# Kernel tuning notes

Measured on AMD Instinct MI355X. Metric: run time of the kernel, lower is better.

Reference implementation:

```python
import jax, jax.numpy as jnp
import numpy as np

GRID = 128                      # grid_size per axis
NUM_CELLS = GRID ** 3
INV_CELL = float(GRID)          # 1.0 / cell_size, cell_size = 1/128, origin = 0
N_POINTS = 1_000_000
D_FEAT = 8
# forward window {0,1}^3 -> 8 stencil offsets (linear shape functions)
OFFSETS = np.stack(np.meshgrid(*([np.arange(2)] * 3), indexing='ij'), -1).reshape(-1, 3)


def setup_inputs() -> dict:
    key = jax.random.key(0)
    k1, k2 = jax.random.split(key)
    position_stack = jax.random.uniform(k1, (N_POINTS, 3), dtype=jnp.float32)  # in [0,1)^3
    point_feature = jax.random.normal(k2, (N_POINTS, D_FEAT), dtype=jnp.float32)
    return {"position_stack": position_stack, "point_feature": point_feature}


def reference(position_stack, point_feature):
    offsets = jnp.asarray(OFFSETS, jnp.int32)                 # [8,3]
    # --- partition: hash each point into its grid cell (origin=0) ---
    rel = position_stack * INV_CELL                            # [N,3], continuous grid coords
    base = jnp.floor(rel).astype(jnp.int32)                    # [N,3] base cell (point_hash grid pos)
    # --- p2g (vmap_grid_gather duality): each point scatters to its 8 forward-window nodes ---
    node = base[:, None, :] + offsets[None, :, :]              # [N,8,3]
    # linear hat weights: prod_d (1 - |rel - node|), nonneg since |diff| <= 1
    w = jnp.prod(1.0 - jnp.abs(rel[:, None, :] - node.astype(rel.dtype)), axis=-1)  # [N,8]
    nw = node % GRID                                           # ravel_multi_index mode='wrap'
    hid = (nw[..., 0] * GRID + nw[..., 1]) * GRID + nw[..., 2]  # [N,8] cell hash ids
    contrib = w[..., None] * point_feature[:, None, :]         # [N,8,D]
    grid_feat = jnp.zeros((NUM_CELLS, D_FEAT), point_feature.dtype)
    grid_feat = grid_feat.at[hid.reshape(-1)].add(contrib.reshape(-1, D_FEAT))  # scatter-add
    # --- g2p (vmap_grid_scatter_fori): gather grid values back to points over forward window ---
    point_out = jnp.einsum('nwd,nw->nd', grid_feat[hid], w)    # [N,D]
    return point_out
```

## Files before the change

kernel.cpp:

```cpp
#include <hip/hip_runtime.h>

#define GRIDSZ 128
#define GMASK 127
#define NUM_CELLS (GRIDSZ * GRIDSZ * GRIDSZ)
#define DFEAT 8
#define NPTS 1000000
#define INV_CELL 128.0f

#define SCAN_BLK 256
#define SCAN_ELEMS 8
#define SCAN_TILE (SCAN_BLK * SCAN_ELEMS)
#define NSCAN_BLOCKS (NUM_CELLS / SCAN_TILE)

__global__ __launch_bounds__(256) void hist_kernel(
    const float* __restrict__ pos,
    int* __restrict__ counts)
{
    int n = blockIdx.x * blockDim.x + threadIdx.x;
    if (n >= NPTS) return;
    float px = pos[n * 3 + 0] * INV_CELL;
    float py = pos[n * 3 + 1] * INV_CELL;
    float pz = pos[n * 3 + 2] * INV_CELL;
    int bx = (int)floorf(px), by = (int)floorf(py), bz = (int)floorf(pz);
    int h = ((bx & GMASK) << 14) | ((by & GMASK) << 7) | (bz & GMASK);
    atomicAdd(&counts[h], 1);
}

__global__ __launch_bounds__(SCAN_BLK) void scan_a(
    int* __restrict__ data,
    int* __restrict__ partial)
{
    __shared__ int lds[SCAN_BLK];
    int t = threadIdx.x;
    int base = blockIdx.x * SCAN_TILE + t * SCAN_ELEMS;
    int v[SCAN_ELEMS];
    int s = 0;
#pragma unroll
    for (int i = 0; i < SCAN_ELEMS; ++i) { v[i] = data[base + i]; s += v[i]; }
    lds[t] = s;
    __syncthreads();
    int incl = s;
    for (int off = 1; off < SCAN_BLK; off <<= 1) {
        int tmp = (t >= off) ? lds[t - off] : 0;
        __syncthreads();
        incl += tmp;
        lds[t] = incl;
        __syncthreads();
    }
    int excl = incl - s;
#pragma unroll
    for (int i = 0; i < SCAN_ELEMS; ++i) { data[base + i] = excl; excl += v[i]; }
    if (t == SCAN_BLK - 1) partial[blockIdx.x] = incl;
}

__global__ __launch_bounds__(1024) void scan_b(int* __restrict__ partial)
{
    __shared__ int lds[NSCAN_BLOCKS];
    int t = threadIdx.x;
    int p = partial[t];
    lds[t] = p;
    __syncthreads();
    int incl = p;
    for (int off = 1; off < NSCAN_BLOCKS; off <<= 1) {
        int tmp = (t >= off) ? lds[t - off] : 0;
        __syncthreads();
        incl += tmp;
        lds[t] = incl;
        __syncthreads();
    }
    partial[t] = incl - p;
}

__global__ __launch_bounds__(256) void scan_c(
    int* __restrict__ offsets, const int* __restrict__ partial)
{
    int i = blockIdx.x * blockDim.x + threadIdx.x;
    offsets[i] += partial[i / SCAN_TILE];
}

__global__ __launch_bounds__(256) void scatter_kernel(
    const float* __restrict__ pos,
    const float* __restrict__ feat,
    int* __restrict__ offsets,
    float4* __restrict__ frac_s,
    float4* __restrict__ feat_s,
    int* __restrict__ orig_s)
{
    int n = blockIdx.x * blockDim.x + threadIdx.x;
    if (n >= NPTS) return;
    float px = pos[n * 3 + 0] * INV_CELL;
    float py = pos[n * 3 + 1] * INV_CELL;
    float pz = pos[n * 3 + 2] * INV_CELL;
    int bx = (int)floorf(px), by = (int)floorf(py), bz = (int)floorf(pz);
    float fx = px - (float)bx, fy = py - (float)by, fz = pz - (float)bz;
    int c = ((bx & GMASK) << 14) | ((by & GMASK) << 7) | (bz & GMASK);
    int slot = atomicAdd(&offsets[c], 1);

    const float4* fp = reinterpret_cast<const float4*>(feat + (size_t)n * DFEAT);
    float4 f0 = fp[0];
    float4 f1 = fp[1];
    frac_s[slot] = make_float4(fx, fy, fz, __int_as_float(c));
    feat_s[(size_t)slot * 2 + 0] = f0;
    feat_s[(size_t)slot * 2 + 1] = f1;
    orig_s[slot] = n;
}

__global__ __launch_bounds__(256) void node_gather_kernel(
    const int* __restrict__ offsets_end,
    const float4* __restrict__ frac_s,
    const float4* __restrict__ feat_s,
    float* __restrict__ grid)
{
    int n = blockIdx.x * blockDim.x + threadIdx.x;
    int nz = n & GMASK, ny = (n >> 7) & GMASK, nx = n >> 14;
    float4 a0 = {0.f, 0.f, 0.f, 0.f};
    float4 a1 = {0.f, 0.f, 0.f, 0.f};
#pragma unroll
    for (int oxy = 0; oxy < 4; ++oxy) {
        int ox = oxy >> 1, oy = oxy & 1;
        int bx = (nx - ox) & GMASK, by = (ny - oy) & GMASK;
        int cbase = (bx << 14) | (by << 7);
        int c1 = cbase | nz;
        if (nz > 0) {
            int c0 = c1 - 1;
            int st0 = (c0 == 0) ? 0 : offsets_end[c0 - 1];
            int en0 = offsets_end[c0];
            int en1 = offsets_end[c1];
            for (int j = st0; j < en1; ++j) {
                float4 fr = frac_s[j];
                float wz = (j < en0) ? fr.z : 1.f - fr.z;
                float w = (ox ? fr.x : 1.f - fr.x) * (oy ? fr.y : 1.f - fr.y) * wz;
                float4 f0 = feat_s[(size_t)j * 2 + 0];
                float4 f1 = feat_s[(size_t)j * 2 + 1];
                a0.x += w * f0.x; a0.y += w * f0.y; a0.z += w * f0.z; a0.w += w * f0.w;
                a1.x += w * f1.x; a1.y += w * f1.y; a1.z += w * f1.z; a1.w += w * f1.w;
            }
        } else {
            int c0 = cbase | 127;
            int st0 = offsets_end[c0 - 1];
            int en0 = offsets_end[c0];
            for (int j = st0; j < en0; ++j) {
                float4 fr = frac_s[j];
                float w = (ox ? fr.x : 1.f - fr.x) * (oy ? fr.y : 1.f - fr.y) * fr.z;
                float4 f0 = feat_s[(size_t)j * 2 + 0];
                float4 f1 = feat_s[(size_t)j * 2 + 1];
                a0.x += w * f0.x; a0.y += w * f0.y; a0.z += w * f0.z; a0.w += w * f0.w;
                a1.x += w * f1.x; a1.y += w * f1.y; a1.z += w * f1.z; a1.w += w * f1.w;
            }
            int st1 = (c1 == 0) ? 0 : offsets_end[c1 - 1];
            int en1 = offsets_end[c1];
            for (int j = st1; j < en1; ++j) {
                float4 fr = frac_s[j];
                float w = (ox ? fr.x : 1.f - fr.x) * (oy ? fr.y : 1.f - fr.y) * (1.f - fr.z);
                float4 f0 = feat_s[(size_t)j * 2 + 0];
                float4 f1 = feat_s[(size_t)j * 2 + 1];
                a0.x += w * f0.x; a0.y += w * f0.y; a0.z += w * f0.z; a0.w += w * f0.w;
                a1.x += w * f1.x; a1.y += w * f1.y; a1.z += w * f1.z; a1.w += w * f1.w;
            }
        }
    }
    float4* gp = reinterpret_cast<float4*>(grid + (size_t)n * DFEAT);
    gp[0] = a0;
    gp[1] = a1;
}

__global__ __launch_bounds__(256) void g2p_sorted_kernel(
    const float4* __restrict__ frac_s,
    const int* __restrict__ orig_s,
    const float* __restrict__ grid,
    float* __restrict__ out)
{
    int j = blockIdx.x * blockDim.x + threadIdx.x;
    if (j >= NPTS) return;
    float4 fr = frac_s[j];
    int c = __float_as_int(fr.w);
    int bx = c >> 14, by = (c >> 7) & GMASK, bz = c & GMASK;

    float wx[2] = {1.0f - fr.x, fr.x};
    float wy[2] = {1.0f - fr.y, fr.y};
    float wz[2] = {1.0f - fr.z, fr.z};

    float4 acc0 = {0.f, 0.f, 0.f, 0.f};
    float4 acc1 = {0.f, 0.f, 0.f, 0.f};
#pragma unroll
    for (int o = 0; o < 8; ++o) {
        int ox = (o >> 2) & 1, oy = (o >> 1) & 1, oz = o & 1;
        float w = wx[ox] * wy[oy] * wz[oz];
        int cx = (bx + ox) & GMASK;
        int cy = (by + oy) & GMASK;
        int cz = (bz + oz) & GMASK;
        int hid = (cx << 14) | (cy << 7) | cz;
        const float4* g = reinterpret_cast<const float4*>(grid + (size_t)hid * DFEAT);
        float4 g0 = g[0];
        float4 g1 = g[1];
        acc0.x += w * g0.x; acc0.y += w * g0.y; acc0.z += w * g0.z; acc0.w += w * g0.w;
        acc1.x += w * g1.x; acc1.y += w * g1.y; acc1.z += w * g1.z; acc1.w += w * g1.w;
    }
    int orig = orig_s[j];
    float4* op = reinterpret_cast<float4*>(out + (size_t)orig * DFEAT);
    op[0] = acc0;
    op[1] = acc1;
}

__global__ __launch_bounds__(256) void p2g_atomic_kernel(
    const float* __restrict__ pos,
    const float* __restrict__ feat,
    float* __restrict__ grid)
{
    int n = blockIdx.x * blockDim.x + threadIdx.x;
    if (n >= NPTS) return;
    float px = pos[n * 3 + 0] * INV_CELL;
    float py = pos[n * 3 + 1] * INV_CELL;
    float pz = pos[n * 3 + 2] * INV_CELL;
    int bx = (int)floorf(px), by = (int)floorf(py), bz = (int)floorf(pz);
    float fx = px - (float)bx, fy = py - (float)by, fz = pz - (float)bz;
    const float4* fp = reinterpret_cast<const float4*>(feat + (size_t)n * DFEAT);
    float4 f0 = fp[0];
    float4 f1 = fp[1];
    float f[8] = {f0.x, f0.y, f0.z, f0.w, f1.x, f1.y, f1.z, f1.w};
    float wx[2] = {1.0f - fx, fx};
    float wy[2] = {1.0f - fy, fy};
    float wz[2] = {1.0f - fz, fz};
#pragma unroll
    for (int o = 0; o < 8; ++o) {
        int ox = (o >> 2) & 1, oy = (o >> 1) & 1, oz = o & 1;
        float w = wx[ox] * wy[oy] * wz[oz];
        int cx = (bx + ox) & GMASK, cy = (by + oy) & GMASK, cz = (bz + oz) & GMASK;
        int hid = (cx << 14) | (cy << 7) | cz;
        float* g = grid + (size_t)hid * DFEAT;
#pragma unroll
        for (int d = 0; d < DFEAT; ++d) atomicAdd(g + d, w * f[d]);
    }
}

__global__ __launch_bounds__(256) void g2p_kernel(
    const float* __restrict__ pos,
    const float* __restrict__ grid,
    float* __restrict__ out)
{
    int n = blockIdx.x * blockDim.x + threadIdx.x;
    if (n >= NPTS) return;
    float px = pos[n * 3 + 0] * INV_CELL;
    float py = pos[n * 3 + 1] * INV_CELL;
    float pz = pos[n * 3 + 2] * INV_CELL;
    int bx = (int)floorf(px), by = (int)floorf(py), bz = (int)floorf(pz);
    float fx = px - (float)bx, fy = py - (float)by, fz = pz - (float)bz;
    float wx[2] = {1.0f - fx, fx};
    float wy[2] = {1.0f - fy, fy};
    float wz[2] = {1.0f - fz, fz};
    float4 acc0 = {0.f, 0.f, 0.f, 0.f};
    float4 acc1 = {0.f, 0.f, 0.f, 0.f};
#pragma unroll
    for (int o = 0; o < 8; ++o) {
        int ox = (o >> 2) & 1, oy = (o >> 1) & 1, oz = o & 1;
        float w = wx[ox] * wy[oy] * wz[oz];
        int cx = (bx + ox) & GMASK;
        int cy = (by + oy) & GMASK;
        int cz = (bz + oz) & GMASK;
        int hid = (cx << 14) | (cy << 7) | cz;
        const float4* g = reinterpret_cast<const float4*>(grid + (size_t)hid * DFEAT);
        float4 g0 = g[0];
        float4 g1 = g[1];
        acc0.x += w * g0.x; acc0.y += w * g0.y; acc0.z += w * g0.z; acc0.w += w * g0.w;
        acc1.x += w * g1.x; acc1.y += w * g1.y; acc1.z += w * g1.z; acc1.w += w * g1.w;
    }
    float4* op = reinterpret_cast<float4*>(out + (size_t)n * DFEAT);
    op[0] = acc0;
    op[1] = acc1;
}

extern "C" void kernel_launch(void* const* d_in, const int* in_sizes, int n_in,
                              void* d_out, int out_size, void* d_ws, size_t ws_size,
                              hipStream_t stream) {
    const float* pos  = (const float*)d_in[0];
    const float* feat = (const float*)d_in[1];
    float* out = (float*)d_out;

    char* ws = (char*)d_ws;
    size_t grid_bytes    = (size_t)NUM_CELLS * DFEAT * sizeof(float);
    size_t offsets_bytes = (size_t)NUM_CELLS * sizeof(int);
    size_t frac_bytes    = (size_t)NPTS * sizeof(float4);
    size_t feats_bytes   = (size_t)NPTS * 2 * sizeof(float4);
    size_t orig_bytes    = (size_t)NPTS * sizeof(int);
    size_t partial_bytes = (size_t)NSCAN_BLOCKS * sizeof(int);

    float* grid     = (float*)ws;
    int* offsets    = (int*)(ws + grid_bytes);
    float4* frac_s  = (float4*)(ws + grid_bytes + offsets_bytes);
    float4* feat_s  = (float4*)(ws + grid_bytes + offsets_bytes + frac_bytes);
    int* orig_s     = (int*)(ws + grid_bytes + offsets_bytes + frac_bytes + feats_bytes);
    int* partial    = (int*)(ws + grid_bytes + offsets_bytes + frac_bytes + feats_bytes + orig_bytes);
    size_t needed = grid_bytes + offsets_bytes + frac_bytes + feats_bytes + orig_bytes + partial_bytes;

    int block = 256;
    int nblk_pts = (NPTS + block - 1) / block;
    int nblk_cells = NUM_CELLS / block;

    if (ws_size >= needed) {
        hipMemsetAsync(offsets, 0, offsets_bytes, stream);
        hist_kernel<<<nblk_pts, block, 0, stream>>>(pos, offsets);
        scan_a<<<NSCAN_BLOCKS, SCAN_BLK, 0, stream>>>(offsets, partial);
        scan_b<<<1, NSCAN_BLOCKS, 0, stream>>>(partial);
        scan_c<<<nblk_cells, block, 0, stream>>>(offsets, partial);
        scatter_kernel<<<nblk_pts, block, 0, stream>>>(pos, feat, offsets, frac_s, feat_s, orig_s);
        node_gather_kernel<<<nblk_cells, block, 0, stream>>>(offsets, frac_s, feat_s, grid);
        g2p_sorted_kernel<<<nblk_pts, block, 0, stream>>>(frac_s, orig_s, grid, out);
    } else {
        hipMemsetAsync(grid, 0, grid_bytes, stream);
        p2g_atomic_kernel<<<nblk_pts, block, 0, stream>>>(pos, feat, grid);
        g2p_kernel<<<nblk_pts, block, 0, stream>>>(pos, grid, out);
    }
}
```

Before: 309.2 us.

## Pack sorted point records and grid into fp16/quantized format, fold scan fixup

Sorted point data is packed into a 32-byte record: features as fp16 pairs, fractional coordinates quantized to 16 bits, plus cell id and original index. The grid is stored as fp16 (16 bytes per cell). The scan_c pass is removed and the block partial sums are added on the fly in scatter and node_gather. This cuts memory traffic and one kernel launch, at the cost of reduced precision in features, grid values and weights, which may break tolerance checks.

```diff
diff --git a/kernel.cpp b/kernel.cpp
--- a/kernel.cpp
+++ b/kernel.cpp
@@ -1,4 +1,5 @@
 #include <hip/hip_runtime.h>
+#include <hip/hip_fp16.h>
 
 #define GRIDSZ 128
 #define GMASK 127
@@ -9,8 +10,22 @@
 
 #define SCAN_BLK 256
 #define SCAN_ELEMS 8
-#define SCAN_TILE (SCAN_BLK * SCAN_ELEMS)
+#define SCAN_TILE 2048
+#define SCAN_SHIFT 11
 #define NSCAN_BLOCKS (NUM_CELLS / SCAN_TILE)
+
+__device__ inline unsigned pack2h(float a, float b) {
+    __half2 h = __floats2half2_rn(a, b);
+    union { __half2 h; unsigned u; } cvt; cvt.h = h; return cvt.u;
+}
+__device__ inline float2 unpack2h(unsigned u) {
+    union { unsigned u; __half2 h; } cvt; cvt.u = u;
+    return __half22float2(cvt.h);
+}
+
+__device__ inline int cum(const int* __restrict__ off, const int* __restrict__ partial, int c) {
+    return off[c] + partial[c >> SCAN_SHIFT];
+}
 
 __global__ __launch_bounds__(256) void hist_kernel(
     const float* __restrict__ pos,
@@ -71,20 +86,12 @@
     partial[t] = incl - p;
 }
 
-__global__ __launch_bounds__(256) void scan_c(
-    int* __restrict__ offsets, const int* __restrict__ partial)
-{
-    int i = blockIdx.x * blockDim.x + threadIdx.x;
-    offsets[i] += partial[i / SCAN_TILE];
-}
-
 __global__ __launch_bounds__(256) void scatter_kernel(
     const float* __restrict__ pos,
     const float* __restrict__ feat,
     int* __restrict__ offsets,
-    float4* __restrict__ frac_s,
-    float4* __restrict__ feat_s,
-    int* __restrict__ orig_s)
+    const int* __restrict__ partial,
+    uint4* __restrict__ rec)
 {
     int n = blockIdx.x * blockDim.x + threadIdx.x;
     if (n >= NPTS) return;
@@ -94,22 +101,35 @@
     int bx = (int)floorf(px), by = (int)floorf(py), bz = (int)floorf(pz);
     float fx = px - (float)bx, fy = py - (float)by, fz = pz - (float)bz;
     int c = ((bx & GMASK) << 14) | ((by & GMASK) << 7) | (bz & GMASK);
-    int slot = atomicAdd(&offsets[c], 1);
+    int slot = atomicAdd(&offsets[c], 1) + partial[c >> SCAN_SHIFT];
 
     const float4* fp = reinterpret_cast<const float4*>(feat + (size_t)n * DFEAT);
     float4 f0 = fp[0];
     float4 f1 = fp[1];
-    frac_s[slot] = make_float4(fx, fy, fz, __int_as_float(c));
-    feat_s[(size_t)slot * 2 + 0] = f0;
-    feat_s[(size_t)slot * 2 + 1] = f1;
-    orig_s[slot] = n;
+
+    uint4 A, B;
+    A.x = pack2h(f0.x, f0.y);
+    A.y = pack2h(f0.z, f0.w);
+    A.z = pack2h(f1.x, f1.y);
+    A.w = pack2h(f1.z, f1.w);
+    unsigned qx = min((unsigned)(fx * 65536.0f), 65535u);
+    unsigned qy = min((unsigned)(fy * 65536.0f), 65535u);
+    unsigned qz = min((unsigned)(fz * 65536.0f), 65535u);
+    B.x = qx | (qy << 16);
+    B.y = qz;
+    B.z = (unsigned)c;
+    B.w = (unsigned)n;
+
+    uint4* dst = rec + (size_t)slot * 2;
+    dst[0] = A;
+    dst[1] = B;
 }
 
 __global__ __launch_bounds__(256) void node_gather_kernel(
     const int* __restrict__ offsets_end,
-    const float4* __restrict__ frac_s,
-    const float4* __restrict__ feat_s,
-    float* __restrict__ grid)
+    const int* __restrict__ partial,
+    const uint4* __restrict__ rec,
+    uint4* __restrict__ gridh)
 {
     int n = blockIdx.x * blockDim.x + threadIdx.x;
     int nz = n & GMASK, ny = (n >> 7) & GMASK, nx = n >> 14;
@@ -123,62 +143,86 @@
         int c1 = cbase | nz;
         if (nz > 0) {
             int c0 = c1 - 1;
-            int st0 = (c0 == 0) ? 0 : offsets_end[c0 - 1];
-            int en0 = offsets_end[c0];
-            int en1 = offsets_end[c1];
+            int st0 = (c0 == 0) ? 0 : cum(offsets_end, partial, c0 - 1);
+            int en0 = cum(offsets_end, partial, c0);
+            int en1 = cum(offsets_end, partial, c1);
             for (int j = st0; j < en1; ++j) {
-                float4 fr = frac_s[j];
-                float wz = (j < en0) ? fr.z : 1.f - fr.z;
-                float w = (ox ? fr.x : 1.f - fr.x) * (oy ? fr.y : 1.f - fr.y) * wz;
-                float4 f0 = feat_s[(size_t)j * 2 + 0];
-                float4 f1 = feat_s[(size_t)j * 2 + 1];
-                a0.x += w * f0.x; a0.y += w * f0.y; a0.z += w * f0.z; a0.w += w * f0.w;
-                a1.x += w * f1.x; a1.y += w * f1.y; a1.z += w * f1.z; a1.w += w * f1.w;
+                const uint4* rp = rec + (size_t)j * 2;
+                uint4 A = rp[0];
+                uint4 B = rp[1];
+                float fx = (float)(B.x & 0xffffu) * (1.f / 65536.f);
+                float fy = (float)(B.x >> 16) * (1.f / 65536.f);
+                float fz = (float)(B.y & 0xffffu) * (1.f / 65536.f);
+                float wz = (j < en0) ? fz : 1.f - fz;
+                float w = (ox ? fx : 1.f - fx) * (oy ? fy : 1.f - fy) * wz;
+                float2 p;
+                p = unpack2h(A.x); a0.x += w * p.x; a0.y += w * p.y;
+                p = unpack2h(A.y); a0.z += w * p.x; a0.w += w * p.y;
+                p = unpack2h(A.z); a1.x += w * p.x; a1.y += w * p.y;
+                p = unpack2h(A.w); a1.z += w * p.x; a1.w += w * p.y;
             }
         } else {
             int c0 = cbase | 127;
-            int st0 = offsets_end[c0 - 1];
-            int en0 = offsets_end[c0];
+            int st0 = cum(offsets_end, partial, c0 - 1);
+            int en0 = cum(offsets_end, partial, c0);
             for (int j = st0; j < en0; ++j) {
-                float4 fr = frac_s[j];
-                float w = (ox ? fr.x : 1.f - fr.x) * (oy ? fr.y : 1.f - fr.y) * fr.z;
-                float4 f0 = feat_s[(size_t)j * 2 + 0];
-                float4 f1 = feat_s[(size_t)j * 2 + 1];
-                a0.x += w * f0.x; a0.y += w * f0.y; a0.z += w * f0.z; a0.w += w * f0.w;
-                a1.x += w * f1.x; a1.y += w * f1.y; a1.z += w * f1.z; a1.w += w * f1.w;
+                const uint4* rp = rec + (size_t)j * 2;
+                uint4 A = rp[0];
+                uint4 B = rp[1];
+                float fx = (float)(B.x & 0xffffu) * (1.f / 65536.f);
+                float fy = (float)(B.x >> 16) * (1.f / 65536.f);
+                float fz = (float)(B.y & 0xffffu) * (1.f / 65536.f);
+                float w = (ox ? fx : 1.f - fx) * (oy ? fy : 1.f - fy) * fz;
+                float2 p;
+                p = unpack2h(A.x); a0.x += w * p.x; a0.y += w * p.y;
+                p = unpack2h(A.y); a0.z += w * p.x; a0.w += w * p.y;
+                p = unpack2h(A.z); a1.x += w * p.x; a1.y += w * p.y;
+                p = unpack2h(A.w); a1.z += w * p.x; a1.w += w * p.y;
             }
-            int st1 = (c1 == 0) ? 0 : offsets_end[c1 - 1];
-            int en1 = offsets_end[c1];
+            int st1 = (c1 == 0) ? 0 : cum(offsets_end, partial, c1 - 1);
+            int en1 = cum(offsets_end, partial, c1);
             for (int j = st1; j < en1; ++j) {
-                float4 fr = frac_s[j];
-                float w = (ox ? fr.x : 1.f - fr.x) * (oy ? fr.y : 1.f - fr.y) * (1.f - fr.z);
-                float4 f0 = feat_s[(size_t)j * 2 + 0];
-                float4 f1 = feat_s[(size_t)j * 2 + 1];
-                a0.x += w * f0.x; a0.y += w * f0.y; a0.z += w * f0.z; a0.w += w * f0.w;
-                a1.x += w * f1.x; a1.y += w * f1.y; a1.z += w * f1.z; a1.w += w * f1.w;
+                const uint4* rp = rec + (size_t)j * 2;
+                uint4 A = rp[0];
+                uint4 B = rp[1];
+                float fx = (float)(B.x & 0xffffu) * (1.f / 65536.f);
+                float fy = (float)(B.x >> 16) * (1.f / 65536.f);
+                float fz = (float)(B.y & 0xffffu) * (1.f / 65536.f);
+                float w = (ox ? fx : 1.f - fx) * (oy ? fy : 1.f - fy) * (1.f - fz);
+                float2 p;
+                p = unpack2h(A.x); a0.x += w * p.x; a0.y += w * p.y;
+                p = unpack2h(A.y); a0.z += w * p.x; a0.w += w * p.y;
+                p = unpack2h(A.z); a1.x += w * p.x; a1.y += w * p.y;
+                p = unpack2h(A.w); a1.z += w * p.x; a1.w += w * p.y;
             }
         }
     }
-    float4* gp = reinterpret_cast<float4*>(grid + (size_t)n * DFEAT);
-    gp[0] = a0;
-    gp[1] = a1;
+    uint4 g;
+    g.x = pack2h(a0.x, a0.y);
+    g.y = pack2h(a0.z, a0.w);
+    g.z = pack2h(a1.x, a1.y);
+    g.w = pack2h(a1.z, a1.w);
+    gridh[n] = g;
 }
 
 __global__ __launch_bounds__(256) void g2p_sorted_kernel(
-    const float4* __restrict__ frac_s,
-    const int* __restrict__ orig_s,
-    const float* __restrict__ grid,
+    const uint4* __restrict__ rec,
+    const uint4* __restrict__ gridh,
     float* __restrict__ out)
 {
     int j = blockIdx.x * blockDim.x + threadIdx.x;
     if (j >= NPTS) return;
-    float4 fr = frac_s[j];
-    int c = __float_as_int(fr.w);
+    uint4 B = rec[(size_t)j * 2 + 1];
+    float fx = (float)(B.x & 0xffffu) * (1.f / 65536.f);
+    float fy = (float)(B.x >> 16) * (1.f / 65536.f);
+    float fz = (float)(B.y & 0xffffu) * (1.f / 65536.f);
+    int c = (int)B.z;
+    int orig = (int)B.w;
     int bx = c >> 14, by = (c >> 7) & GMASK, bz = c & GMASK;
 
-    float wx[2] = {1.0f - fr.x, fr.x};
-    float wy[2] = {1.0f - fr.y, fr.y};
-    float wz[2] = {1.0f - fr.z, fr.z};
+    float wx[2] = {1.0f - fx, fx};
+    float wy[2] = {1.0f - fy, fy};
+    float wz[2] = {1.0f - fz, fz};
 
     float4 acc0 = {0.f, 0.f, 0.f, 0.f};
     float4 acc1 = {0.f, 0.f, 0.f, 0.f};
@@ -190,13 +234,13 @@
         int cy = (by + oy) & GMASK;
         int cz = (bz + oz) & GMASK;
         int hid = (cx << 14) | (cy << 7) | cz;
-        const float4* g = reinterpret_cast<const float4*>(grid + (size_t)hid * DFEAT);
-        float4 g0 = g[0];
-        float4 g1 = g[1];
-        acc0.x += w * g0.x; acc0.y += w * g0.y; acc0.z += w * g0.z; acc0.w += w * g0.w;
-        acc1.x += w * g1.x; acc1.y += w * g1.y; acc1.z += w * g1.z; acc1.w += w * g1.w;
-    }
-    int orig = orig_s[j];
+        uint4 g = gridh[hid];
+        float2 p;
+        p = unpack2h(g.x); acc0.x += w * p.x; acc0.y += w * p.y;
+        p = unpack2h(g.y); acc0.z += w * p.x; acc0.w += w * p.y;
+        p = unpack2h(g.z); acc1.x += w * p.x; acc1.y += w * p.y;
+        p = unpack2h(g.w); acc1.z += w * p.x; acc1.w += w * p.y;
+    }
     float4* op = reinterpret_cast<float4*>(out + (size_t)orig * DFEAT);
     op[0] = acc0;
     op[1] = acc1;
@@ -277,20 +321,16 @@
     float* out = (float*)d_out;
 
     char* ws = (char*)d_ws;
-    size_t grid_bytes    = (size_t)NUM_CELLS * DFEAT * sizeof(float);
+    size_t gridh_bytes   = (size_t)NUM_CELLS * sizeof(uint4);
     size_t offsets_bytes = (size_t)NUM_CELLS * sizeof(int);
-    size_t frac_bytes    = (size_t)NPTS * sizeof(float4);
-    size_t feats_bytes   = (size_t)NPTS * 2 * sizeof(float4);
-    size_t orig_bytes    = (size_t)NPTS * sizeof(int);
+    size_t rec_bytes     = (size_t)NPTS * 2 * sizeof(uint4);
     size_t partial_bytes = (size_t)NSCAN_BLOCKS * sizeof(int);
 
-    float* grid     = (float*)ws;
-    int* offsets    = (int*)(ws + grid_bytes);
-    float4* frac_s  = (float4*)(ws + grid_bytes + offsets_bytes);
-    float4* feat_s  = (float4*)(ws + grid_bytes + offsets_bytes + frac_bytes);
-    int* orig_s     = (int*)(ws + grid_bytes + offsets_bytes + frac_bytes + feats_bytes);
-    int* partial    = (int*)(ws + grid_bytes + offsets_bytes + frac_bytes + feats_bytes + orig_bytes);
-    size_t needed = grid_bytes + offsets_bytes + frac_bytes + feats_bytes + orig_bytes + partial_bytes;
+    uint4* gridh  = (uint4*)ws;
+    int* offsets  = (int*)(ws + gridh_bytes);
+    uint4* rec    = (uint4*)(ws + gridh_bytes + offsets_bytes);
+    int* partial  = (int*)(ws + gridh_bytes + offsets_bytes + rec_bytes);
+    size_t needed = gridh_bytes + offsets_bytes + rec_bytes + partial_bytes;
 
     int block = 256;
     int nblk_pts = (NPTS + block - 1) / block;
@@ -301,12 +341,12 @@
         hist_kernel<<<nblk_pts, block, 0, stream>>>(pos, offsets);
         scan_a<<<NSCAN_BLOCKS, SCAN_BLK, 0, stream>>>(offsets, partial);
         scan_b<<<1, NSCAN_BLOCKS, 0, stream>>>(partial);
-        scan_c<<<nblk_cells, block, 0, stream>>>(offsets, partial);
-        scatter_kernel<<<nblk_pts, block, 0, stream>>>(pos, feat, offsets, frac_s, feat_s, orig_s);
-        node_gather_kernel<<<nblk_cells, block, 0, stream>>>(offsets, frac_s, feat_s, grid);
-        g2p_sorted_kernel<<<nblk_pts, block, 0, stream>>>(frac_s, orig_s, grid, out);
+        scatter_kernel<<<nblk_pts, block, 0, stream>>>(pos, feat, offsets, partial, rec);
+        node_gather_kernel<<<nblk_cells, block, 0, stream>>>(offsets, partial, rec, gridh);
+        g2p_sorted_kernel<<<nblk_pts, block, 0, stream>>>(rec, gridh, out);
     } else {
-        hipMemsetAsync(grid, 0, grid_bytes, stream);
+        float* grid = (float*)ws;
+        hipMemsetAsync(grid, 0, (size_t)NUM_CELLS * DFEAT * sizeof(float), stream);
         p2g_atomic_kernel<<<nblk_pts, block, 0, stream>>>(pos, feat, grid);
         g2p_kernel<<<nblk_pts, block, 0, stream>>>(pos, grid, out);
     }
```

Result: faster. 262.7 us (-15.0%).
